# Kernel tuning notes

Measured on AMD Instinct MI355X. Metric: run time of the kernel, lower is better.

The kernel has to match this reference:

```python
import jax, jax.numpy as jnp
import numpy as np

S, B_BOX, N_CLASS = 7, 2, 20
L_COORD, L_NOOBJ = 5.0, 0.5
BATCH = 4096
C = 5 * B_BOX + N_CLASS  # 30


def setup_inputs() -> dict:
    key = jax.random.key(0)
    k1, k2, k3, k4 = jax.random.split(key, 4)
    # coords/w/h/classes strictly positive (sqrt is applied to raw values)
    y = jax.random.uniform(k1, (BATCH, S, S, C), minval=0.05, maxval=0.95, dtype=jnp.float32)
    # confidence channels must be exactly 0/1 (mask tests == 1)
    conf0 = jax.random.bernoulli(k3, 0.3, (BATCH, S, S)).astype(jnp.float32)
    conf1 = jax.random.bernoulli(k4, 0.3, (BATCH, S, S)).astype(jnp.float32)
    y = y.at[..., 0].set(conf0).at[..., 5].set(conf1)
    y_h = jax.random.uniform(k2, (BATCH, S, S, C), minval=0.05, maxval=0.95, dtype=jnp.float32)
    return {"y": y, "y_h": y_h}


def _loss(y, y_h):
    b_sz = y.shape[0]
    conf_idx = np.arange(B_BOX) * 5  # [0, 5]
    y_conf = y[..., conf_idx]        # [B,S,S,b]
    yh_conf = y_h[..., conf_idx]
    mf = (y_conf == 1.0).astype(y.dtype)  # obj mask per box, constant wrt grads
    dconf = (y_conf - yh_conf) ** 2
    loss_obj = jnp.sum(dconf * mf)
    loss_noobj = jnp.sum(dconf * (1.0 - mf))

    loss_coord = jnp.zeros((), y.dtype)
    loss_prob = jnp.zeros((), y.dtype)
    for k in range(B_BOX):  # static small loop over boxes
        mk = mf[..., k]  # [B,S,S]
        base = 5 * k
        dxy = (y[..., base + 1] - y_h[..., base + 1]) ** 2 \
            + (y[..., base + 2] - y_h[..., base + 2]) ** 2
        dwh = (jnp.sqrt(y[..., base + 3]) - jnp.sqrt(y_h[..., base + 3])) ** 2 \
            + (jnp.sqrt(y[..., base + 4]) - jnp.sqrt(y_h[..., base + 4])) ** 2
        loss_coord = loss_coord + jnp.sum((dxy + dwh) * mk)

        # prob term: slice from k*5+5 to end (faithful to original, for k=0 this
        # includes box-2's 5 entries), softmax over the masked batch dimension.
        tail = y[..., base + 5:]
        tail_h = y_h[..., base + 5:]
        mkb = mk[..., None]  # [B,S,S,1]
        neg = jnp.where(mkb > 0, tail_h, -jnp.inf)
        m = jnp.max(neg, axis=0)                       # [S,S,Ct]
        m_safe = jnp.where(jnp.isfinite(m), m, 0.0)    # guard empty columns
        p = jnp.exp(tail_h - m_safe) * mkb
        denom = jnp.sum(p, axis=0)
        sm = p / jnp.where(denom > 0, denom, 1.0)
        loss_prob = loss_prob + jnp.sum((tail - sm) ** 2 * mkb)

    loss = loss_obj + L_NOOBJ * loss_noobj + L_COORD * loss_coord + loss_prob
    return loss / b_sz


def reference(y, y_h):
    return _loss(y, y_h)
```

## Files before the change

### kernel.cpp

```cpp
#include <hip/hip_runtime.h>
#include <math.h>

#define CC 30
#define NBATCH 4096
#define NIJ 49
#define NPAIR 1225
#define NSLOT6 7350
#define THREADS 512


__global__ __launch_bounds__(THREADS)
void yolo_main(const float* __restrict__ y, const float* __restrict__ yh,
               float* __restrict__ scal, float* __restrict__ parts, int nwg)
{
    __shared__ float tY[4 * 1470];
    __shared__ float tH[4 * 1470];
    __shared__ float scr[4][8];

    const int tid = threadIdx.x;
    const int wg  = blockIdx.x;
    const int bpw = NBATCH / nwg;
    const int nslab = bpw >> 2;

    int  ijv[3], cv[3], pr[3];
    bool val[3];
    #pragma unroll
    for (int i = 0; i < 3; i++) {
        int p = tid + i * THREADS;
        val[i] = (p < NPAIR);
        pr[i]  = p;
        int pp = val[i] ? p : 0;
        ijv[i] = pp / 25;
        cv[i]  = 5 + pp % 25;
    }

    float D0[3] = {0,0,0}, B0[3] = {0,0,0}, C0[3] = {0,0,0};
    float D1[3] = {0,0,0}, B1[3] = {0,0,0}, C1[3] = {0,0,0};
    float obj = 0.f, noobj = 0.f, coord = 0.f, tt = 0.f;

    for (int s = 0; s < nslab; s++) {
        const int b0 = wg * bpw + s * 4;
        const size_t f4 = (size_t)b0 * 1470 / 4;
        const float4* Y4 = (const float4*)y  + f4;
        const float4* H4 = (const float4*)yh + f4;
        float4* tY4 = (float4*)tY;
        float4* tH4 = (float4*)tH;
        #pragma unroll 3
        for (int i = tid; i < 1470; i += THREADS) { tY4[i] = Y4[i]; tH4[i] = H4[i]; }
        __syncthreads();

        if (tid < 4 * NIJ) {
            const int base = tid * CC;
            float y0 = tY[base],     h0 = tH[base];
            float y5 = tY[base + 5], h5 = tH[base + 5];
            float d0 = y0 - h0; d0 *= d0;
            float d5 = y5 - h5; d5 *= d5;
            const bool m0 = (y0 == 1.0f), m1 = (y5 == 1.0f);
            obj   += (m0 ? d0 : 0.f) + (m1 ? d5 : 0.f);
            noobj += (m0 ? 0.f : d0) + (m1 ? 0.f : d5);
            if (m0) {
                float a  = tY[base + 1] - tH[base + 1];
                float b2 = tY[base + 2] - tH[base + 2];
                float c1 = sqrtf(tY[base + 3]) - sqrtf(tH[base + 3]);
                float c2 = sqrtf(tY[base + 4]) - sqrtf(tH[base + 4]);
                coord += a * a + b2 * b2 + c1 * c1 + c2 * c2;
            }
            if (m1) {
                float a  = tY[base + 6] - tH[base + 6];
                float b2 = tY[base + 7] - tH[base + 7];
                float c1 = sqrtf(tY[base + 8]) - sqrtf(tH[base + 8]);
                float c2 = sqrtf(tY[base + 9]) - sqrtf(tH[base + 9]);
                coord += a * a + b2 * b2 + c1 * c1 + c2 * c2;
            }
        }

        #pragma unroll
        for (int b = 0; b < 4; b++) {
            #pragma unroll
            for (int i = 0; i < 3; i++) {
                if (!val[i]) continue;
                const int cb = b * 1470 + ijv[i] * CC;
                const float w0 = (tY[cb] == 1.0f) ? 1.f : 0.f;
                const float w1 = (cv[i] >= 10 && tY[cb + 5] == 1.0f) ? 1.f : 0.f;
                const float t  = tY[cb + cv[i]];
                const float th = tH[cb + cv[i]];
                const float e  = __expf(th);
                const float te = t * e, ee = e * e, t2 = t * t;
                D0[i] = fmaf(e,  w0, D0[i]);
                B0[i] = fmaf(te, w0, B0[i]);
                C0[i] = fmaf(ee, w0, C0[i]);
                D1[i] = fmaf(e,  w1, D1[i]);
                B1[i] = fmaf(te, w1, B1[i]);
                C1[i] = fmaf(ee, w1, C1[i]);
                tt = fmaf(t2, w0 + w1, tt);
            }
        }
        __syncthreads();
    }

    float* pp = parts + (size_t)wg * NSLOT6;
    #pragma unroll
    for (int i = 0; i < 3; i++) {
        if (!val[i]) continue;
        const int p = pr[i];
        pp[p]            = D0[i];
        pp[NPAIR + p]    = B0[i];
        pp[2*NPAIR + p]  = C0[i];
        pp[3*NPAIR + p]  = D1[i];
        pp[4*NPAIR + p]  = B1[i];
        pp[5*NPAIR + p]  = C1[i];
    }

    const int lane = tid & 63, wv = tid >> 6;
    #pragma unroll
    for (int off = 32; off > 0; off >>= 1) {
        obj   += __shfl_down(obj,   off);
        noobj += __shfl_down(noobj, off);
        coord += __shfl_down(coord, off);
        tt    += __shfl_down(tt,    off);
    }
    if (lane == 0) { scr[0][wv] = obj; scr[1][wv] = noobj; scr[2][wv] = coord; scr[3][wv] = tt; }
    __syncthreads();
    if (tid < 4) {
        float sacc = 0.f;
        #pragma unroll
        for (int w = 0; w < THREADS / 64; w++) sacc += scr[tid][w];
        scal[wg * 4 + tid] = sacc;
    }
}

__global__ __launch_bounds__(1024)
void yolo_reduce(const float* __restrict__ parts, float* __restrict__ tbl, int nwg)
{
    const int pl = threadIdx.x & 127;
    const int ch = threadIdx.x >> 7;
    const int p  = blockIdx.x * 128 + pl;
    const int per = nwg >> 3;
    float s = 0.f;
    if (p < NSLOT6) {
        const float* q = parts + (size_t)(ch * per) * NSLOT6 + p;
        #pragma unroll 4
        for (int w = 0; w < per; ++w) { s += *q; q += NSLOT6; }
    }
    __shared__ float sred[8][128];
    sred[ch][pl] = s;
    __syncthreads();
    if (threadIdx.x < 128) {
        const int pp = blockIdx.x * 128 + threadIdx.x;
        if (pp < NSLOT6) {
            float t = 0.f;
            #pragma unroll
            for (int c = 0; c < 8; c++) t += sred[c][threadIdx.x];
            tbl[pp] = t;
        }
    }
}

__global__ __launch_bounds__(1024)
void yolo_final(const float* __restrict__ tbl, const float* __restrict__ scal,
                float* __restrict__ out, int nwg)
{
    float v = 0.f;

    for (int s = threadIdx.x; s < NPAIR; s += 1024) {
        const int cidx = s % 25;
        float D0 = tbl[s], B0 = tbl[NPAIR + s], C0 = tbl[2*NPAIR + s];
        if (D0 > 0.f) v += C0 / (D0 * D0) - 2.f * B0 / D0;
        if (cidx >= 5) {
            float D1 = tbl[3*NPAIR + s], B1 = tbl[4*NPAIR + s], C1 = tbl[5*NPAIR + s];
            if (D1 > 0.f) v += C1 / (D1 * D1) - 2.f * B1 / D1;
        }
    }

    const float4* s4 = (const float4*)scal;
    for (int w = threadIdx.x; w < nwg; w += 1024) {
        float4 a = s4[w];
        v += a.x + 0.5f * a.y + 5.0f * a.z + a.w;
    }

    __shared__ float sred[16];
    #pragma unroll
    for (int off = 32; off > 0; off >>= 1) v += __shfl_down(v, off);
    const int lane = threadIdx.x & 63, wv = threadIdx.x >> 6;
    if (lane == 0) sred[wv] = v;
    __syncthreads();
    if (threadIdx.x == 0) {
        float tot = 0.f;
        #pragma unroll
        for (int w = 0; w < 16; w++) tot += sred[w];
        out[0] = tot / (float)NBATCH;
    }
}

extern "C" void kernel_launch(void* const* d_in, const int* in_sizes, int n_in,
                              void* d_out, int out_size, void* d_ws, size_t ws_size,
                              hipStream_t stream)
{
    const float* y  = (const float*)d_in[0];
    const float* yh = (const float*)d_in[1];
    float* out   = (float*)d_out;
    float* tbl   = (float*)d_ws;
    float* scal  = (float*)((char*)d_ws + 29696);
    float* parts = (float*)((char*)d_ws + 38912);

    const size_t per_wg = (size_t)NSLOT6 * sizeof(float);
    int nwg;
    if      (ws_size >= 38912 + 512 * per_wg) nwg = 512;
    else if (ws_size >= 38912 + 256 * per_wg) nwg = 256;
    else if (ws_size >= 38912 + 128 * per_wg) nwg = 128;
    else                                      nwg = 64;

    yolo_main<<<nwg, THREADS, 0, stream>>>(y, yh, scal, parts, nwg);
    yolo_reduce<<<(NSLOT6 + 127) / 128, 1024, 0, stream>>>(parts, tbl, nwg);
    yolo_final<<<1, 1024, 0, stream>>>(tbl, scal, out, nwg);
}
```

Before: 31.59 us.

## Prefetch next slab into registers and restructure the partial-sum reduction

The main kernel now loads the next 4-batch slab from global memory into registers while it computes on the current slab in LDS, then writes the registers to LDS after a barrier. This is meant to hide global load latency behind compute. The cross-workgroup reduction is reworked: partials are padded to a float4-aligned stride, the reduce kernel uses a 2D grid that emits 8 partial tables, and the final kernel sums those 8. The maximum workgroup count drops from 512 to 256. Together these raise per-WG work while shrinking the reduction traffic, at the cost of an extra barrier per slab and extra register pressure.

```diff
diff --git a/kernel.cpp b/kernel.cpp
--- a/kernel.cpp
+++ b/kernel.cpp
@@ -5,8 +5,9 @@
 #define NBATCH 4096
 #define NIJ 49
 #define NPAIR 1225
-#define NSLOT6 7350
+#define PSTR 7352
 #define THREADS 512
+#define SLABF4 1470
 
 
 __global__ __launch_bounds__(THREADS)
@@ -21,6 +22,11 @@
     const int wg  = blockIdx.x;
     const int bpw = NBATCH / nwg;
     const int nslab = bpw >> 2;
+
+    const int i0 = tid, i1 = tid + 512;
+    const int i2r = tid + 1024;
+    const int i2  = (i2r < SLABF4) ? i2r : (SLABF4 - 1);
+    const bool w2 = (i2r < SLABF4);
 
     int  ijv[3], cv[3], pr[3];
     bool val[3];
@@ -38,16 +44,28 @@
     float D1[3] = {0,0,0}, B1[3] = {0,0,0}, C1[3] = {0,0,0};
     float obj = 0.f, noobj = 0.f, coord = 0.f, tt = 0.f;
 
+    const float4* Yg = (const float4*)y;
+    const float4* Hg = (const float4*)yh;
+    float4* tY4 = (float4*)tY;
+    float4* tH4 = (float4*)tH;
+
+    {
+        const size_t f4 = (size_t)((wg * bpw) >> 2) * SLABF4;
+        float4 a0 = Yg[f4+i0], a1 = Yg[f4+i1], a2 = Yg[f4+i2];
+        float4 b0 = Hg[f4+i0], b1 = Hg[f4+i1], b2 = Hg[f4+i2];
+        tY4[i0] = a0; tY4[i1] = a1; if (w2) tY4[i2] = a2;
+        tH4[i0] = b0; tH4[i1] = b1; if (w2) tH4[i2] = b2;
+    }
+    __syncthreads();
+
+    float4 ry0, ry1, ry2, rh0, rh1, rh2;
+
     for (int s = 0; s < nslab; s++) {
-        const int b0 = wg * bpw + s * 4;
-        const size_t f4 = (size_t)b0 * 1470 / 4;
-        const float4* Y4 = (const float4*)y  + f4;
-        const float4* H4 = (const float4*)yh + f4;
-        float4* tY4 = (float4*)tY;
-        float4* tH4 = (float4*)tH;
-        #pragma unroll 3
-        for (int i = tid; i < 1470; i += THREADS) { tY4[i] = Y4[i]; tH4[i] = H4[i]; }
-        __syncthreads();
+        if (s + 1 < nslab) {
+            const size_t nf4 = (size_t)((wg * bpw + (s+1)*4) >> 2) * SLABF4;
+            ry0 = Yg[nf4+i0]; ry1 = Yg[nf4+i1]; ry2 = Yg[nf4+i2];
+            rh0 = Hg[nf4+i0]; rh1 = Hg[nf4+i1]; rh2 = Hg[nf4+i2];
+        }
 
         if (tid < 4 * NIJ) {
             const int base = tid * CC;
@@ -96,9 +114,14 @@
             }
         }
         __syncthreads();
-    }
-
-    float* pp = parts + (size_t)wg * NSLOT6;
+        if (s + 1 < nslab) {
+            tY4[i0] = ry0; tY4[i1] = ry1; if (w2) tY4[i2] = ry2;
+            tH4[i0] = rh0; tH4[i1] = rh1; if (w2) tH4[i2] = rh2;
+        }
+        __syncthreads();
+    }
+
+    float* pp = parts + (size_t)wg * PSTR;
     #pragma unroll
     for (int i = 0; i < 3; i++) {
         if (!val[i]) continue;
@@ -129,47 +152,56 @@
     }
 }
 
+__global__ __launch_bounds__(512)
+void yolo_reduce(const float* __restrict__ parts, float* __restrict__ parts2, int nwg)
+{
+    const int lane = threadIdx.x & 63;
+    const int sub  = threadIdx.x >> 6;
+    const int f4i  = blockIdx.x * 64 + lane;
+    const int cy   = blockIdx.y;
+    const int wpc  = nwg >> 3;
+    const int wps  = wpc >> 3;
+
+    float4 s = make_float4(0.f, 0.f, 0.f, 0.f);
+    if (f4i < PSTR / 4) {
+        const float* q = parts + (size_t)(cy * wpc + sub * wps) * PSTR + f4i * 4;
+        for (int w = 0; w < wps; ++w) {
+            float4 a = *(const float4*)q;
+            s.x += a.x; s.y += a.y; s.z += a.z; s.w += a.w;
+            q += PSTR;
+        }
+    }
+    __shared__ float4 sred[8][64];
+    sred[sub][lane] = s;
+    __syncthreads();
+    if (threadIdx.x < 64 && f4i < PSTR / 4) {
+        float4 t = sred[0][lane];
+        #pragma unroll
+        for (int c = 1; c < 8; c++) {
+            float4 a = sred[c][lane];
+            t.x += a.x; t.y += a.y; t.z += a.z; t.w += a.w;
+        }
+        *(float4*)(parts2 + (size_t)cy * PSTR + f4i * 4) = t;
+    }
+}
+
 __global__ __launch_bounds__(1024)
-void yolo_reduce(const float* __restrict__ parts, float* __restrict__ tbl, int nwg)
-{
-    const int pl = threadIdx.x & 127;
-    const int ch = threadIdx.x >> 7;
-    const int p  = blockIdx.x * 128 + pl;
-    const int per = nwg >> 3;
-    float s = 0.f;
-    if (p < NSLOT6) {
-        const float* q = parts + (size_t)(ch * per) * NSLOT6 + p;
-        #pragma unroll 4
-        for (int w = 0; w < per; ++w) { s += *q; q += NSLOT6; }
-    }
-    __shared__ float sred[8][128];
-    sred[ch][pl] = s;
-    __syncthreads();
-    if (threadIdx.x < 128) {
-        const int pp = blockIdx.x * 128 + threadIdx.x;
-        if (pp < NSLOT6) {
-            float t = 0.f;
-            #pragma unroll
-            for (int c = 0; c < 8; c++) t += sred[c][threadIdx.x];
-            tbl[pp] = t;
-        }
-    }
-}
-
-__global__ __launch_bounds__(1024)
-void yolo_final(const float* __restrict__ tbl, const float* __restrict__ scal,
+void yolo_final(const float* __restrict__ parts2, const float* __restrict__ scal,
                 float* __restrict__ out, int nwg)
 {
     float v = 0.f;
 
     for (int s = threadIdx.x; s < NPAIR; s += 1024) {
         const int cidx = s % 25;
-        float D0 = tbl[s], B0 = tbl[NPAIR + s], C0 = tbl[2*NPAIR + s];
+        float D0 = 0, B0 = 0, C0 = 0, D1 = 0, B1 = 0, C1 = 0;
+        #pragma unroll
+        for (int c = 0; c < 8; c++) {
+            const float* t = parts2 + (size_t)c * PSTR;
+            D0 += t[s];           B0 += t[NPAIR + s];   C0 += t[2*NPAIR + s];
+            D1 += t[3*NPAIR + s]; B1 += t[4*NPAIR + s]; C1 += t[5*NPAIR + s];
+        }
         if (D0 > 0.f) v += C0 / (D0 * D0) - 2.f * B0 / D0;
-        if (cidx >= 5) {
-            float D1 = tbl[3*NPAIR + s], B1 = tbl[4*NPAIR + s], C1 = tbl[5*NPAIR + s];
-            if (D1 > 0.f) v += C1 / (D1 * D1) - 2.f * B1 / D1;
-        }
+        if (cidx >= 5 && D1 > 0.f) v += C1 / (D1 * D1) - 2.f * B1 / D1;
     }
 
     const float4* s4 = (const float4*)scal;
@@ -198,19 +230,19 @@
 {
     const float* y  = (const float*)d_in[0];
     const float* yh = (const float*)d_in[1];
-    float* out   = (float*)d_out;
-    float* tbl   = (float*)d_ws;
-    float* scal  = (float*)((char*)d_ws + 29696);
-    float* parts = (float*)((char*)d_ws + 38912);
-
-    const size_t per_wg = (size_t)NSLOT6 * sizeof(float);
+    float* out    = (float*)d_out;
+    float* scal   = (float*)d_ws;
+    float* parts2 = (float*)((char*)d_ws + 4096);
+    float* parts  = (float*)((char*)d_ws + 239616);
+
+    const size_t per_wg = (size_t)PSTR * sizeof(float);
     int nwg;
-    if      (ws_size >= 38912 + 512 * per_wg) nwg = 512;
-    else if (ws_size >= 38912 + 256 * per_wg) nwg = 256;
-    else if (ws_size >= 38912 + 128 * per_wg) nwg = 128;
-    else                                      nwg = 64;
+    if      (ws_size >= 239616 + 256 * per_wg) nwg = 256;
+    else if (ws_size >= 239616 + 128 * per_wg) nwg = 128;
+    else                                       nwg = 64;
 
     yolo_main<<<nwg, THREADS, 0, stream>>>(y, yh, scal, parts, nwg);
-    yolo_reduce<<<(NSLOT6 + 127) / 128, 1024, 0, stream>>>(parts, tbl, nwg);
-    yolo_final<<<1, 1024, 0, stream>>>(tbl, scal, out, nwg);
-}
+    dim3 g2((PSTR / 4 + 63) / 64, 8);
+    yolo_reduce<<<g2, 512, 0, stream>>>(parts, parts2, nwg);
+    yolo_final<<<1, 1024, 0, stream>>>(parts2, scal, out, nwg);
+}
```

Result: faster. 27.87 us (-11.8%).
